# Performance work log

Hardware: AMD Instinct MI355X
Metric: run time of the kernel (lower is better)

The kernel has to match this reference:

```python
import jax, jax.numpy as jnp
import numpy as np

B, C, H, W = 4, 64, 64, 64
NH = 1            # num_heads
HD = C // NH      # head dim
HID = 256         # mlp hidden = 4*dim
EPS = 1e-5


def _gn(x, g, b):
    # GroupNorm with num_groups=1: normalize over (C,H,W) per sample
    mu = x.mean(axis=(1, 2, 3), keepdims=True)
    var = ((x - mu) ** 2).mean(axis=(1, 2, 3), keepdims=True)
    xn = (x - mu) / jnp.sqrt(var + EPS)
    return xn * g[None, :, None, None] + b[None, :, None, None]


def _bn(x, g, b):
    # BatchNorm2d eval mode, running_mean=0, running_var=1
    s = g / jnp.sqrt(1.0 + EPS)
    return x * s[None, :, None, None] + b[None, :, None, None]


def _c1(x, w):
    # 1x1 conv, no bias
    return jnp.einsum('oc,bchw->bohw', w, x)


def _dw(x, w, b):
    # depthwise conv, kernel k, 'same' padding
    k = w.shape[-1]
    p = k // 2
    y = jax.lax.conv_general_dilated(
        x, w, (1, 1), [(p, p), (p, p)],
        dimension_numbers=('NCHW', 'OIHW', 'NCHW'),
        feature_group_count=x.shape[1])
    return y + b[None, :, None, None]


def _rope_sincos():
    d = HD
    angle = 1.0 / 10000 ** jnp.linspace(0.0, 1.0, d // 4)
    angle = jnp.repeat(angle, 2)  # [d/2]
    th = jnp.arange(H, dtype=jnp.float32)[:, None] * angle[None, :]
    tw = jnp.arange(W, dtype=jnp.float32)[:, None] * angle[None, :]
    sin = jnp.concatenate([
        jnp.broadcast_to(jnp.sin(th)[:, None, :], (H, W, d // 2)),
        jnp.broadcast_to(jnp.sin(tw)[None, :, :], (H, W, d // 2))], -1)
    cos = jnp.concatenate([
        jnp.broadcast_to(jnp.cos(th)[:, None, :], (H, W, d // 2)),
        jnp.broadcast_to(jnp.cos(tw)[None, :, :], (H, W, d // 2))], -1)
    return sin.reshape(H * W, d), cos.reshape(H * W, d)


def _rot(x):
    x1 = x[..., ::2]
    x2 = x[..., 1::2]
    return jnp.stack([-x2, x1], axis=-1).reshape(x.shape)


def _theta_shift(x, sin, cos):
    return x * cos + _rot(x) * sin


def _forward(x, cnn_feature, n1_g, n1_b, n2_g, n2_b, n3_g, n3_b,
             q_w, q_b, kv_w, kv_b, lc_w, lc_b,
             fc1_w, bn1_g, bn1_b,
             dw_w1, dw_b1, dw_w3, dw_b3, dw_w5, dw_b5, dw_w7, dw_b7,
             bnm_g, bnm_b, fft_w, fc2_w, bn2_g, bn2_b):
    N = H * W
    sin, cos = _rope_sincos()
    # ---- attention branch ----
    xn = _gn(x, n1_g, n1_b)
    cn = _gn(cnn_feature, n3_g, n3_b)
    q = (_c1(xn, q_w) + q_b[None, :, None, None]).reshape(B, NH, HD, N).transpose(0, 1, 3, 2)
    kv_in = _dw(cn, lc_w, lc_b) + cn          # local_conv(kv) + kv
    kv = _c1(kv_in, kv_w) + kv_b[None, :, None, None]
    k, v = jnp.split(kv, 2, axis=1)
    k = k.reshape(B, NH, HD, N).transpose(0, 1, 3, 2)  # [B,h,N,d]
    v = v.reshape(B, NH, HD, N).transpose(0, 1, 3, 2)
    qr = _theta_shift(q, sin, cos)
    kr = _theta_shift(k, sin, cos)
    attn = jnp.einsum('bhnd,bhmd->bhnm', qr, kr) * (HD ** -0.5)
    attn = jax.nn.softmax(attn, axis=-1)
    o = jnp.einsum('bhnm,bhmd->bhnd', attn, v)
    o = o.transpose(0, 1, 3, 2).reshape(B, C, H, W)
    x = x + o
    # ---- fft MLP branch ----
    xn2 = _gn(x, n2_g, n2_b)
    h = jax.nn.gelu(_bn(_c1(xn2, fc1_w), bn1_g, bn1_b), approximate=False)
    res = h
    c0 = HID - (HID // 4) * 3
    s1, s3, s5, s7 = jnp.split(h, [c0, c0 + HID // 4, c0 + 2 * (HID // 4)], axis=1)
    hd = jnp.concatenate([_dw(s1, dw_w1, dw_b1), _dw(s3, dw_w3, dw_b3),
                          _dw(s5, dw_w5, dw_b5), _dw(s7, dw_w7, dw_b7)], axis=1)
    pad = 0 if W % 2 == 0 else (W // 2 + 1) * 2 - W
    hp = jnp.pad(hd, ((0, 0), (0, 0), (0, 0), (0, pad)))
    hf = jnp.fft.rfft2(hp)
    hf = fft_w * hf
    hp = jnp.fft.irfft2(hf, s=hp.shape[-2:])
    hd = hp[..., :W]
    h = hd + res
    h = _bn(jax.nn.gelu(h, approximate=False), bnm_g, bnm_b)
    out = _bn(_c1(h, fc2_w), bn2_g, bn2_b)
    return x + out


def setup_inputs() -> dict:
    key = jax.random.key(0)
    ks = jax.random.split(key, 16)
    def rn(i, shape, s=0.02):
        return jax.random.normal(ks[i], shape, jnp.float32) * s
    c4 = HID // 4
    c0 = HID - 3 * c4
    return {
        'x': jax.random.normal(ks[0], (B, C, H, W), jnp.float32),
        'cnn_feature': jax.random.normal(ks[1], (B, C, H, W), jnp.float32),
        'n1_g': jnp.ones((C,)), 'n1_b': jnp.zeros((C,)),
        'n2_g': jnp.ones((C,)), 'n2_b': jnp.zeros((C,)),
        'n3_g': jnp.ones((C,)), 'n3_b': jnp.zeros((C,)),
        'q_w': rn(2, (C, C)), 'q_b': jnp.zeros((C,)),
        'kv_w': rn(3, (2 * C, C)), 'kv_b': jnp.zeros((2 * C,)),
        'lc_w': rn(4, (C, 1, 3, 3)), 'lc_b': jnp.zeros((C,)),
        'fc1_w': rn(5, (HID, C)),
        'bn1_g': jnp.ones((HID,)), 'bn1_b': jnp.zeros((HID,)),
        'dw_w1': rn(6, (c0, 1, 1, 1)), 'dw_b1': jnp.zeros((c0,)),
        'dw_w3': rn(7, (c4, 1, 3, 3)), 'dw_b3': jnp.zeros((c4,)),
        'dw_w5': rn(8, (c4, 1, 5, 5)), 'dw_b5': jnp.zeros((c4,)),
        'dw_w7': rn(9, (c4, 1, 7, 7)), 'dw_b7': jnp.zeros((c4,)),
        'bnm_g': jnp.ones((HID,)), 'bnm_b': jnp.zeros((HID,)),
        'fft_w': jax.random.normal(ks[10], (1, HID, 1, 1), jnp.float32),
        'fc2_w': rn(11, (C, HID)),
        'bn2_g': jnp.ones((C,)), 'bn2_b': jnp.zeros((C,)),
    }


def reference(x, cnn_feature, n1_g, n1_b, n2_g, n2_b, n3_g, n3_b,
              q_w, q_b, kv_w, kv_b, lc_w, lc_b,
              fc1_w, bn1_g, bn1_b,
              dw_w1, dw_b1, dw_w3, dw_b3, dw_w5, dw_b5, dw_w7, dw_b7,
              bnm_g, bnm_b, fft_w, fc2_w, bn2_g, bn2_b):
    return _forward(x, cnn_feature, n1_g, n1_b, n2_g, n2_b, n3_g, n3_b,
                    q_w, q_b, kv_w, kv_b, lc_w, lc_b,
                    fc1_w, bn1_g, bn1_b,
                    dw_w1, dw_b1, dw_w3, dw_b3, dw_w5, dw_b5, dw_w7, dw_b7,
                    bnm_g, bnm_b, fft_w, fc2_w, bn2_g, bn2_b)
```

## Files before the change

kernel.cpp:

```cpp
#include <hip/hip_runtime.h>
#include <hip/hip_bf16.h>
#include <math.h>

#define BB 4
#define CC 64
#define NN 4096
#define HD 64
#define HID 256
#define EPSV 1e-5f
#define CNT (CC*NN)
#define NCH 8

typedef float f32x4 __attribute__((ext_vector_type(4)));
typedef short bf16x8 __attribute__((ext_vector_type(8)));
typedef short bf16x4 __attribute__((ext_vector_type(4)));
#define MFMA16(a, b, c) __builtin_amdgcn_mfma_f32_16x16x32_bf16(a, b, c, 0, 0, 0)

__device__ __forceinline__ float gelu_exact(float x) {
    return 0.5f * x * (1.0f + erff(x * 0.70710678118654752f));
}
__device__ __forceinline__ ushort f2bf(float f) {
    unsigned u = __float_as_uint(f);
    unsigned r = (u + 0x7FFFu + ((u >> 16) & 1u)) >> 16;
    return (ushort)r;
}
__device__ __forceinline__ float bf2f(ushort u) {
    return __uint_as_float(((unsigned)u) << 16);
}
__device__ __forceinline__ unsigned cvtpk(float lo, float hi) {
    unsigned r;
    asm("v_cvt_pk_bf16_f32 %0, %1, %2" : "=v"(r) : "v"(lo), "v"(hi));
    return r;
}
__device__ __forceinline__ void unpack2(unsigned u, float& lo, float& hi) {
    lo = __uint_as_float(u << 16);
    hi = __uint_as_float(u & 0xffff0000u);
}

__global__ __launch_bounds__(256) void wprep_kernel(const float* __restrict__ fc1w,
                                                    const float* __restrict__ fc2w,
                                                    const float* __restrict__ qw,
                                                    const float* __restrict__ kvw,
                                                    ushort* __restrict__ fc1wb,
                                                    ushort* __restrict__ fc2wb,
                                                    ushort* __restrict__ qwb,
                                                    ushort* __restrict__ kvwb) {
    int i = blockIdx.x * 256 + threadIdx.x;
    if (i < 16384) fc1wb[i] = f2bf(fc1w[i]);
    else if (i < 32768) fc2wb[i - 16384] = f2bf(fc2w[i - 16384]);
    else if (i < 36864) qwb[i - 32768] = f2bf(qw[i - 32768]);
    else if (i < 45056) kvwb[i - 36864] = f2bf(kvw[i - 36864]);
}

__global__ __launch_bounds__(256) void stats_pair_kernel(const float* __restrict__ x,
                                                         const float* __restrict__ cnn,
                                                         float* __restrict__ part) {
    int b = blockIdx.y;
    int blk = blockIdx.x;
    const float4* p0 = (const float4*)(x + (size_t)b * CNT);
    const float4* p1 = (const float4*)(cnn + (size_t)b * CNT);
    float s0 = 0.f, s20 = 0.f, s1 = 0.f, s21 = 0.f;
    #pragma unroll
    for (int k = 0; k < 4; ++k) {
        float4 v = p0[blk * 1024 + k * 256 + threadIdx.x];
        s0  += v.x + v.y + v.z + v.w;
        s20 += v.x * v.x + v.y * v.y + v.z * v.z + v.w * v.w;
        float4 u = p1[blk * 1024 + k * 256 + threadIdx.x];
        s1  += u.x + u.y + u.z + u.w;
        s21 += u.x * u.x + u.y * u.y + u.z * u.z + u.w * u.w;
    }
    #pragma unroll
    for (int off = 32; off > 0; off >>= 1) {
        s0  += __shfl_xor(s0, off);
        s20 += __shfl_xor(s20, off);
        s1  += __shfl_xor(s1, off);
        s21 += __shfl_xor(s21, off);
    }
    __shared__ float sh[4][4];
    int wid = threadIdx.x >> 6, lane = threadIdx.x & 63;
    if (lane == 0) { sh[wid][0] = s0; sh[wid][1] = s20; sh[wid][2] = s1; sh[wid][3] = s21; }
    __syncthreads();
    if (threadIdx.x == 0) {
        float a0 = sh[0][0] + sh[1][0] + sh[2][0] + sh[3][0];
        float a1 = sh[0][1] + sh[1][1] + sh[2][1] + sh[3][1];
        float a2 = sh[0][2] + sh[1][2] + sh[2][2] + sh[3][2];
        float a3 = sh[0][3] + sh[1][3] + sh[2][3] + sh[3][3];
        part[((0 * 4 + b) * 64 + blk) * 2]     = a0;
        part[((0 * 4 + b) * 64 + blk) * 2 + 1] = a1;
        part[((1 * 4 + b) * 64 + blk) * 2]     = a2;
        part[((1 * 4 + b) * 64 + blk) * 2 + 1] = a3;
    }
}

__global__ __launch_bounds__(64) void stats_fin_kernel(const float* __restrict__ part,
                                                       float* __restrict__ stats) {
    int sb_ = blockIdx.x;
    int lane = threadIdx.x;
    float s = part[(sb_ * 64 + lane) * 2];
    float s2 = part[(sb_ * 64 + lane) * 2 + 1];
    #pragma unroll
    for (int off = 32; off > 0; off >>= 1) {
        s  += __shfl_xor(s, off);
        s2 += __shfl_xor(s2, off);
    }
    if (lane == 0) {
        int slot = sb_ >> 2, b = sb_ & 3;
        float mu = s / (float)CNT;
        float var = s2 / (float)CNT - mu * mu;
        stats[slot * 8 + b] = mu;
        stats[slot * 8 + 4 + b] = rsqrtf(var + EPSV);
    }
}

__global__ __launch_bounds__(256) void stats2b_kernel(const float* __restrict__ part2,
                                                      float* __restrict__ stats, int slot) {
    int b = blockIdx.x;
    int t = threadIdx.x;
    float s = part2[(b * 256 + t) * 2];
    float s2 = part2[(b * 256 + t) * 2 + 1];
    #pragma unroll
    for (int off = 32; off > 0; off >>= 1) {
        s  += __shfl_xor(s, off);
        s2 += __shfl_xor(s2, off);
    }
    __shared__ float shs[4], shs2[4];
    int wid = t >> 6, lane = t & 63;
    if (lane == 0) { shs[wid] = s; shs2[wid] = s2; }
    __syncthreads();
    if (t == 0) {
        float S = shs[0] + shs[1] + shs[2] + shs[3];
        float S2 = shs2[0] + shs2[1] + shs2[2] + shs2[3];
        float mu = S / (float)CNT;
        float var = S2 / (float)CNT - mu * mu;
        stats[slot * 8 + b] = mu;
        stats[slot * 8 + 4 + b] = rsqrtf(var + EPSV);
    }
}

__global__ __launch_bounds__(256) void dw3k_kernel(const float* __restrict__ cnn,
                                                   const float* __restrict__ n3g,
                                                   const float* __restrict__ n3b,
                                                   const float* __restrict__ lcw,
                                                   const float* __restrict__ lcb,
                                                   const float* __restrict__ stats,
                                                   float* __restrict__ kvin) {
    int i = blockIdx.x * 256 + threadIdx.x;
    int x = i & 63;
    int y = (i >> 6) & 63;
    int c = (i >> 12) & 63;
    int b = i >> 18;
    float mu = stats[1 * 8 + b];
    float rs = stats[1 * 8 + 4 + b];
    float sc = rs * n3g[c];
    float of = n3b[c] - mu * sc;
    const float* plane = cnn + ((size_t)(i >> 12) << 12);
    float acc = lcb[c];
    #pragma unroll
    for (int dy = 0; dy < 3; ++dy) {
        int yy = y + dy - 1;
        if (yy < 0 || yy >= 64) continue;
        #pragma unroll
        for (int dx = 0; dx < 3; ++dx) {
            int xx = x + dx - 1;
            if (xx < 0 || xx >= 64) continue;
            acc += lcw[c * 9 + dy * 3 + dx] * (plane[(yy << 6) + xx] * sc + of);
        }
    }
    kvin[i] = acc + plane[(y << 6) + x] * sc + of;
}

__global__ __launch_bounds__(256) void q_mfma(const float* __restrict__ x,
                                              const float* __restrict__ n1g,
                                              const float* __restrict__ n1b,
                                              const ushort* __restrict__ qwb,
                                              const float* __restrict__ qb,
                                              const float* __restrict__ stats,
                                              ushort* __restrict__ qr) {
    int b = blockIdx.y;
    int tok0 = blockIdx.x * 64;
    int tid = threadIdx.x;
    int w = tid >> 6;
    int lr = tid & 15;
    int lg = (tid & 63) >> 4;
    float mu = stats[0 * 8 + b];
    float rs = stats[0 * 8 + 4 + b];
    __shared__ ushort Xt[64][64];
    for (int k = 0; k < 16; ++k) {
        int e = tid + k * 256;
        int c = e >> 6, t = e & 63;
        float v = (x[((size_t)(b * 64 + c)) * NN + tok0 + t] - mu) * rs * n1g[c] + n1b[c];
        Xt[t][((c >> 3) ^ (t & 7)) * 8 + (c & 7)] = f2bf(v);
    }
    __syncthreads();
    int brow = w * 16 + lr;
    bf16x8 bf0 = *(const bf16x8*)&Xt[brow][((0 + lg) ^ (lr & 7)) * 8];
    bf16x8 bf1 = *(const bf16x8*)&Xt[brow][((4 + lg) ^ (lr & 7)) * 8];
    f32x4 acc[4];
    #pragma unroll
    for (int mt = 0; mt < 4; ++mt) acc[mt] = (f32x4){0.f, 0.f, 0.f, 0.f};
    #pragma unroll
    for (int mt = 0; mt < 4; ++mt) {
        bf16x8 a0 = *(const bf16x8*)&qwb[(mt * 16 + lr) * 64 + lg * 8];
        bf16x8 a1 = *(const bf16x8*)&qwb[(mt * 16 + lr) * 64 + 32 + lg * 8];
        acc[mt] = MFMA16(a0, bf0, acc[mt]);
        acc[mt] = MFMA16(a1, bf1, acc[mt]);
    }
    int tok = tok0 + w * 16 + lr;
    int hh = tok >> 6, ww2 = tok & 63;
    ushort* qrow = qr + ((size_t)b * NN + tok) * 64;
    #pragma unroll
    for (int mt = 0; mt < 4; ++mt) {
        #pragma unroll
        for (int pr = 0; pr < 2; ++pr) {
            int o = mt * 16 + lg * 4 + pr * 2;
            float a0 = acc[mt][pr * 2]     + qb[o];
            float a1 = acc[mt][pr * 2 + 1] + qb[o + 1];
            int j = (o & 31) >> 1;
            float freq = exp2f(-0.88584749f * (float)j);
            float pos = (o < 32) ? (float)hh : (float)ww2;
            float st, ct;
            __sincosf(pos * freq, &st, &ct);
            qrow[o]     = f2bf(a0 * ct - a1 * st);
            qrow[o + 1] = f2bf(a1 * ct + a0 * st);
        }
    }
}

__global__ __launch_bounds__(256) void kv_mfma(const float* __restrict__ kvin,
                                               const ushort* __restrict__ kvwb,
                                               const float* __restrict__ kvb,
                                               ushort* __restrict__ kr,
                                               ushort* __restrict__ vt) {
    int b = blockIdx.y;
    int tok0 = blockIdx.x * 64;
    int tid = threadIdx.x;
    int w = tid >> 6;
    int lr = tid & 15;
    int lg = (tid & 63) >> 4;
    __shared__ ushort Xt[64][64];
    for (int k = 0; k < 16; ++k) {
        int e = tid + k * 256;
        int c = e >> 6, t = e & 63;
        Xt[t][((c >> 3) ^ (t & 7)) * 8 + (c & 7)] =
            f2bf(kvin[((size_t)(b * 64 + c)) * NN + tok0 + t]);
    }
    __syncthreads();
    int brow = w * 16 + lr;
    bf16x8 bf0 = *(const bf16x8*)&Xt[brow][((0 + lg) ^ (lr & 7)) * 8];
    bf16x8 bf1 = *(const bf16x8*)&Xt[brow][((4 + lg) ^ (lr & 7)) * 8];
    f32x4 acc[8];
    #pragma unroll
    for (int mt = 0; mt < 8; ++mt) acc[mt] = (f32x4){0.f, 0.f, 0.f, 0.f};
    #pragma unroll
    for (int mt = 0; mt < 8; ++mt) {
        bf16x8 a0 = *(const bf16x8*)&kvwb[(mt * 16 + lr) * 64 + lg * 8];
        bf16x8 a1 = *(const bf16x8*)&kvwb[(mt * 16 + lr) * 64 + 32 + lg * 8];
        acc[mt] = MFMA16(a0, bf0, acc[mt]);
        acc[mt] = MFMA16(a1, bf1, acc[mt]);
    }
    int tl = w * 16 + lr;
    int tok = tok0 + tl;
    int hh = tok >> 6, ww2 = tok & 63;
    int permk = (lr >> 2) * 16 + w * 4 + (lr & 3);
    ushort* krow = kr + ((size_t)b * NN + tok) * 64;
    #pragma unroll
    for (int mt = 0; mt < 4; ++mt) {
        #pragma unroll
        for (int pr = 0; pr < 2; ++pr) {
            int o = mt * 16 + lg * 4 + pr * 2;
            float a0 = acc[mt][pr * 2]     + kvb[o];
            float a1 = acc[mt][pr * 2 + 1] + kvb[o + 1];
            int j = (o & 31) >> 1;
            float freq = exp2f(-0.88584749f * (float)j);
            float pos = (o < 32) ? (float)hh : (float)ww2;
            float st, ct;
            __sincosf(pos * freq, &st, &ct);
            krow[o]     = f2bf(a0 * ct - a1 * st);
            krow[o + 1] = f2bf(a1 * ct + a0 * st);
        }
    }
    #pragma unroll
    for (int mt = 4; mt < 8; ++mt) {
        #pragma unroll
        for (int r = 0; r < 4; ++r) {
            int o = mt * 16 + lg * 4 + r;
            float a0 = acc[mt][r] + kvb[o];
            vt[((size_t)b * 64 + (o - 64)) * NN + tok0 + permk] = f2bf(a0);
        }
    }
}

__global__ __launch_bounds__(256) void attn_kernel(const ushort* __restrict__ qr,
                                                   const ushort* __restrict__ kr,
                                                   const ushort* __restrict__ vt,
                                                   ushort* __restrict__ Opart,
                                                   float* __restrict__ ml) {
    int b = blockIdx.y;
    int q0 = blockIdx.x * 64;
    int chunk = blockIdx.z;
    int tid = threadIdx.x;
    int w = tid >> 6;
    int lane = tid & 63;
    int lr = lane & 15;
    int lg = lane >> 4;
    const float SCL2 = 0.125f * 1.44269504f;

    __shared__ ushort Kl[64 * 64];
    __shared__ ushort Vl[64 * 64];

    bf16x8 qf[2];
    {
        const ushort* qp = qr + ((size_t)b * NN + q0 + w * 16 + lr) * 64;
        qf[0] = *(const bf16x8*)(qp + lg * 8);
        qf[1] = *(const bf16x8*)(qp + 32 + lg * 8);
    }

    f32x4 oacc[4];
    #pragma unroll
    for (int t = 0; t < 4; ++t) oacc[t] = (f32x4){0.f, 0.f, 0.f, 0.f};
    float m_ = -INFINITY, l_ = 0.f;

    const size_t kbase = ((size_t)b * NN) * 64;
    const int t0 = chunk * 8, tend = t0 + 8;

    for (int t = t0; t < tend; ++t) {
        int k0 = t * 64;
        __syncthreads();
        #pragma unroll
        for (int it = 0; it < 2; ++it) {
            int e = tid + it * 256;
            int row = e >> 3, cib = e & 7;
            int sw = cib ^ (row & 7);
            *(bf16x8*)(Kl + row * 64 + sw * 8) =
                *(const bf16x8*)(kr + kbase + (size_t)(k0 + row) * 64 + cib * 8);
            *(bf16x8*)(Vl + row * 64 + sw * 8) =
                *(const bf16x8*)(vt + ((size_t)b * 64 + row) * NN + k0 + cib * 8);
        }
        __syncthreads();

        f32x4 sacc[4];
        #pragma unroll
        for (int kt = 0; kt < 4; ++kt) {
            int row = kt * 16 + lr;
            bf16x8 k0f = *(const bf16x8*)(Kl + row * 64 + ((0 * 4 + lg) ^ (lr & 7)) * 8);
            bf16x8 k1f = *(const bf16x8*)(Kl + row * 64 + ((1 * 4 + lg) ^ (lr & 7)) * 8);
            f32x4 z = {0.f, 0.f, 0.f, 0.f};
            z = MFMA16(k0f, qf[0], z);
            sacc[kt] = MFMA16(k1f, qf[1], z);
        }

        float vmax = fmaxf(fmaxf(fmaxf(sacc[0][0], sacc[0][1]), fmaxf(sacc[0][2], sacc[0][3])),
                           fmaxf(fmaxf(sacc[1][0], sacc[1][1]), fmaxf(sacc[1][2], sacc[1][3])));
        vmax = fmaxf(vmax, fmaxf(fmaxf(fmaxf(sacc[2][0], sacc[2][1]), fmaxf(sacc[2][2], sacc[2][3])),
                                 fmaxf(fmaxf(sacc[3][0], sacc[3][1]), fmaxf(sacc[3][2], sacc[3][3]))));
        vmax = fmaxf(vmax, __shfl_xor(vmax, 16));
        vmax = fmaxf(vmax, __shfl_xor(vmax, 32));
        float mx = vmax * SCL2;
        if (__any(mx - m_ > 8.f)) {
            float mn = fmaxf(m_, mx);
            float cr = exp2f(m_ - mn);
            l_ *= cr;
            m_ = mn;
            float crq[4];
            #pragma unroll
            for (int r = 0; r < 4; ++r) crq[r] = __shfl(cr, lg * 4 + r);
            #pragma unroll
            for (int ht = 0; ht < 4; ++ht)
                #pragma unroll
                for (int r = 0; r < 4; ++r) oacc[ht][r] *= crq[r];
        }

        unsigned u[8];
        float lsum = 0.f;
        #pragma unroll
        for (int kt = 0; kt < 4; ++kt) {
            float p0 = exp2f(sacc[kt][0] * SCL2 - m_);
            float p1 = exp2f(sacc[kt][1] * SCL2 - m_);
            float p2 = exp2f(sacc[kt][2] * SCL2 - m_);
            float p3 = exp2f(sacc[kt][3] * SCL2 - m_);
            lsum += (p0 + p1) + (p2 + p3);
            u[kt * 2]     = cvtpk(p0, p1);
            u[kt * 2 + 1] = cvtpk(p2, p3);
        }
        lsum += __shfl_xor(lsum, 16);
        lsum += __shfl_xor(lsum, 32);
        l_ += lsum;

        uint4 t0v = {u[0], u[1], u[2], u[3]};
        uint4 t1v = {u[4], u[5], u[6], u[7]};
        bf16x8 pa0 = __builtin_bit_cast(bf16x8, t0v);
        bf16x8 pa1 = __builtin_bit_cast(bf16x8, t1v);
        #pragma unroll
        for (int ht = 0; ht < 4; ++ht) {
            int row = ht * 16 + lr;
            bf16x8 vf0 = *(const bf16x8*)(Vl + row * 64 + ((lg * 2) ^ (row & 7)) * 8);
            bf16x8 vf1 = *(const bf16x8*)(Vl + row * 64 + ((lg * 2 + 1) ^ (row & 7)) * 8);
            oacc[ht] = MFMA16(pa0, vf0, oacc[ht]);
            oacc[ht] = MFMA16(pa1, vf1, oacc[ht]);
        }
    }

    int n0 = q0 + w * 16 + lg * 4;
    #pragma unroll
    for (int ht = 0; ht < 4; ++ht) {
        int hd = ht * 16 + lr;
        ushort4 o4;
        o4.x = f2bf(oacc[ht][0]);
        o4.y = f2bf(oacc[ht][1]);
        o4.z = f2bf(oacc[ht][2]);
        o4.w = f2bf(oacc[ht][3]);
        *(ushort4*)&Opart[(((size_t)chunk * BB + b) * 64 + hd) * NN + n0] = o4;
    }
    if (lg == 0) {
        int n = q0 + w * 16 + lr;
        ml[((size_t)b * NN + n) * 16 + chunk * 2]     = m_;
        ml[((size_t)b * NN + n) * 16 + chunk * 2 + 1] = l_;
    }
}

__global__ __launch_bounds__(256) void combine_kernel(const ushort* __restrict__ Opart,
                                                      const float* __restrict__ ml,
                                                      const float* __restrict__ x,
                                                      float* __restrict__ x2,
                                                      float* __restrict__ part2) {
    int i = blockIdx.x * 256 + threadIdx.x;
    int n4 = i & 1023;
    int hd = (i >> 10) & 63;
    int b = i >> 16;
    int n0 = n4 << 2;
    float wgt[4][NCH];
    const float* mlp = ml + ((size_t)b * NN + n0) * 16;
    #pragma unroll
    for (int tk = 0; tk < 4; ++tk) {
        float m[NCH], l[NCH];
        const float4* p4 = (const float4*)(mlp + tk * 16);
        #pragma unroll
        for (int q = 0; q < 4; ++q) {
            float4 v = p4[q];
            m[q * 2] = v.x; l[q * 2] = v.y; m[q * 2 + 1] = v.z; l[q * 2 + 1] = v.w;
        }
        float M = m[0];
        #pragma unroll
        for (int c = 1; c < NCH; ++c) M = fmaxf(M, m[c]);
        float e[NCH], L = 0.f;
        #pragma unroll
        for (int c = 0; c < NCH; ++c) { e[c] = exp2f(m[c] - M); L += l[c] * e[c]; }
        float inv = 1.f / L;
        #pragma unroll
        for (int c = 0; c < NCH; ++c) wgt[tk][c] = e[c] * inv;
    }
    float4 acc = {0.f, 0.f, 0.f, 0.f};
    #pragma unroll
    for (int c = 0; c < NCH; ++c) {
        ushort4 o4 = *(const ushort4*)&Opart[(((size_t)c * BB + b) * 64 + hd) * NN + n0];
        acc.x += bf2f(o4.x) * wgt[0][c];
        acc.y += bf2f(o4.y) * wgt[1][c];
        acc.z += bf2f(o4.z) * wgt[2][c];
        acc.w += bf2f(o4.w) * wgt[3][c];
    }
    size_t off = ((size_t)b * 64 + hd) * NN + n0;
    float4 xv = *(const float4*)&x[off];
    acc.x += xv.x; acc.y += xv.y; acc.z += xv.z; acc.w += xv.w;
    *(float4*)&x2[off] = acc;

    float s = acc.x + acc.y + acc.z + acc.w;
    float s2 = acc.x * acc.x + acc.y * acc.y + acc.z * acc.z + acc.w * acc.w;
    #pragma unroll
    for (int off2 = 32; off2 > 0; off2 >>= 1) {
        s  += __shfl_xor(s, off2);
        s2 += __shfl_xor(s2, off2);
    }
    __shared__ float shs[4], shs2[4];
    int wid = threadIdx.x >> 6, lane = threadIdx.x & 63;
    if (lane == 0) { shs[wid] = s; shs2[wid] = s2; }
    __syncthreads();
    if (threadIdx.x == 0) {
        part2[blockIdx.x * 2]     = shs[0] + shs[1] + shs[2] + shs[3];
        part2[blockIdx.x * 2 + 1] = shs2[0] + shs2[1] + shs2[2] + shs2[3];
    }
}

__global__ __launch_bounds__(256) void fc1_mfma(const float* __restrict__ x2,
                                                const ushort* __restrict__ fc1wb,
                                                const float* __restrict__ n2g,
                                                const float* __restrict__ n2b,
                                                const float* __restrict__ bn1g,
                                                const float* __restrict__ bn1b,
                                                const float* __restrict__ stats,
                                                ushort* __restrict__ h1) {
    int b = blockIdx.y;
    int tok0 = (blockIdx.x >> 1) * 64;
    int half = blockIdx.x & 1;
    int tid = threadIdx.x;
    int w = tid >> 6;
    int lr = tid & 15;
    int lg = (tid & 63) >> 4;
    float mu = stats[2 * 8 + b];
    float rs = stats[2 * 8 + 4 + b];
    __shared__ ushort Xt[64][64];
    for (int k = 0; k < 16; ++k) {
        int e = tid + k * 256;
        int c = e >> 6, t = e & 63;
        float v = (x2[((size_t)(b * 64 + c)) * NN + tok0 + t] - mu) * rs * n2g[c] + n2b[c];
        Xt[t][((c >> 3) ^ (t & 7)) * 8 + (c & 7)] = f2bf(v);
    }
    __syncthreads();
    int brow = w * 16 + lr;
    bf16x8 bf0 = *(const bf16x8*)&Xt[brow][((0 + lg) ^ (lr & 7)) * 8];
    bf16x8 bf1 = *(const bf16x8*)&Xt[brow][((4 + lg) ^ (lr & 7)) * 8];
    f32x4 acc[8];
    #pragma unroll
    for (int mt = 0; mt < 8; ++mt) acc[mt] = (f32x4){0.f, 0.f, 0.f, 0.f};
    const ushort* wb = fc1wb + (size_t)(half * 128) * 64;
    #pragma unroll
    for (int mt = 0; mt < 8; ++mt) {
        bf16x8 a0 = *(const bf16x8*)&wb[(mt * 16 + lr) * 64 + lg * 8];
        bf16x8 a1 = *(const bf16x8*)&wb[(mt * 16 + lr) * 64 + 32 + lg * 8];
        acc[mt] = MFMA16(a0, bf0, acc[mt]);
        acc[mt] = MFMA16(a1, bf1, acc[mt]);
    }
    const float sb = rsqrtf(1.f + EPSV);
    int tok = tok0 + w * 16 + lr;
    #pragma unroll
    for (int mt = 0; mt < 8; ++mt) {
        #pragma unroll
        for (int r = 0; r < 4; ++r) {
            int o = half * 128 + mt * 16 + lg * 4 + r;
            float vv = acc[mt][r] * bn1g[o] * sb + bn1b[o];
            h1[((size_t)b * HID + o) * NN + tok] = f2bf(gelu_exact(vv));
        }
    }
}

__global__ __launch_bounds__(256) void mixer_kernel(const ushort* __restrict__ h1,
                                                    const float* __restrict__ dw1w, const float* __restrict__ dw1b,
                                                    const float* __restrict__ dw3w, const float* __restrict__ dw3b,
                                                    const float* __restrict__ dw5w, const float* __restrict__ dw5b,
                                                    const float* __restrict__ dw7w, const float* __restrict__ dw7b,
                                                    const float* __restrict__ fftw,
                                                    const float* __restrict__ bnmg, const float* __restrict__ bnmb,
                                                    ushort* __restrict__ h2) {
    int c = blockIdx.x >> 1;
    int r0 = (blockIdx.x & 1) * 32;
    int b = blockIdx.y;
    int tid = threadIdx.x;
    __shared__ ushort ls[38][80];
    uint* lz = (uint*)&ls[0][0];
    #pragma unroll
    for (int k = 0; k < 6; ++k) {
        int i = tid + k * 256;
        if (i < 1520) lz[i] = 0;
    }
    __syncthreads();
    const ushort* plane = h1 + (((size_t)b * HID + c) << 12);
    for (int e = tid; e < 304; e += 256) {
        int i = e >> 3, xc = e & 7;
        int gr = r0 + i - 3;
        if (gr >= 0 && gr < 64) {
            bf16x8 v = *(const bf16x8*)&plane[(gr << 6) + xc * 8];
            bf16x4 lo = {v[0], v[1], v[2], v[3]};
            bf16x4 hi = {v[4], v[5], v[6], v[7]};
            *(bf16x4*)&ls[i][xc * 8 + 4] = lo;
            *(bf16x4*)&ls[i][xc * 8 + 8] = hi;
        }
    }
    __syncthreads();

    int yy = tid >> 3;
    int x0 = (tid & 7) * 8;
    const float sb = rsqrtf(1.f + EPSV);
    float fw = fftw[c];
    float bg = bnmg[c] * sb, bb2 = bnmb[c];
    float acc[8], ctr[8];
    #pragma unroll
    for (int j = 0; j < 8; ++j) acc[j] = 0.f;

    if (c < 64) {
        float w0 = dw1w[c], b0 = dw1b[c];
        uint4 ua = *(const uint4*)&ls[yy + 3][x0];
        uint4 ub = *(const uint4*)&ls[yy + 3][x0 + 8];
        float wv[16];
        unpack2(ua.x, wv[0], wv[1]); unpack2(ua.y, wv[2], wv[3]);
        unpack2(ua.z, wv[4], wv[5]); unpack2(ua.w, wv[6], wv[7]);
        unpack2(ub.x, wv[8], wv[9]); unpack2(ub.y, wv[10], wv[11]);
        unpack2(ub.z, wv[12], wv[13]); unpack2(ub.w, wv[14], wv[15]);
        #pragma unroll
        for (int j = 0; j < 8; ++j) { ctr[j] = wv[j + 4]; acc[j] = w0 * ctr[j] + b0; }
    } else if (c < 128) {
        int lc = c - 64;
        float b0 = dw3b[lc];
        #pragma unroll
        for (int j = 0; j < 8; ++j) acc[j] = b0;
        #pragma unroll
        for (int dy = 0; dy < 3; ++dy) {
            int i = yy + dy + 2;
            uint4 ua = *(const uint4*)&ls[i][x0];
            uint4 ub = *(const uint4*)&ls[i][x0 + 8];
            float wv[16];
            unpack2(ua.x, wv[0], wv[1]); unpack2(ua.y, wv[2], wv[3]);
            unpack2(ua.z, wv[4], wv[5]); unpack2(ua.w, wv[6], wv[7]);
            unpack2(ub.x, wv[8], wv[9]); unpack2(ub.y, wv[10], wv[11]);
            unpack2(ub.z, wv[12], wv[13]); unpack2(ub.w, wv[14], wv[15]);
            if (dy == 1) {
                #pragma unroll
                for (int j = 0; j < 8; ++j) ctr[j] = wv[j + 4];
            }
            #pragma unroll
            for (int dx = 0; dx < 3; ++dx) {
                float wt = dw3w[lc * 9 + dy * 3 + dx];
                #pragma unroll
                for (int j = 0; j < 8; ++j) acc[j] += wt * wv[j + dx + 3];
            }
        }
    } else if (c < 192) {
        int lc = c - 128;
        float b0 = dw5b[lc];
        #pragma unroll
        for (int j = 0; j < 8; ++j) acc[j] = b0;
        #pragma unroll
        for (int dy = 0; dy < 5; ++dy) {
            int i = yy + dy + 1;
            uint4 ua = *(const uint4*)&ls[i][x0];
            uint4 ub = *(const uint4*)&ls[i][x0 + 8];
            float wv[16];
            unpack2(ua.x, wv[0], wv[1]); unpack2(ua.y, wv[2], wv[3]);
            unpack2(ua.z, wv[4], wv[5]); unpack2(ua.w, wv[6], wv[7]);
            unpack2(ub.x, wv[8], wv[9]); unpack2(ub.y, wv[10], wv[11]);
            unpack2(ub.z, wv[12], wv[13]); unpack2(ub.w, wv[14], wv[15]);
            if (dy == 2) {
                #pragma unroll
                for (int j = 0; j < 8; ++j) ctr[j] = wv[j + 4];
            }
            #pragma unroll
            for (int dx = 0; dx < 5; ++dx) {
                float wt = dw5w[lc * 25 + dy * 5 + dx];
                #pragma unroll
                for (int j = 0; j < 8; ++j) acc[j] += wt * wv[j + dx + 2];
            }
        }
    } else {
        int lc = c - 192;
        float b0 = dw7b[lc];
        #pragma unroll
        for (int j = 0; j < 8; ++j) acc[j] = b0;
        #pragma unroll
        for (int dy = 0; dy < 7; ++dy) {
            int i = yy + dy;
            uint4 ua = *(const uint4*)&ls[i][x0];
            uint4 ub = *(const uint4*)&ls[i][x0 + 8];
            float wv[16];
            unpack2(ua.x, wv[0], wv[1]); unpack2(ua.y, wv[2], wv[3]);
            unpack2(ua.z, wv[4], wv[5]); unpack2(ua.w, wv[6], wv[7]);
            unpack2(ub.x, wv[8], wv[9]); unpack2(ub.y, wv[10], wv[11]);
            unpack2(ub.z, wv[12], wv[13]); unpack2(ub.w, wv[14], wv[15]);
            if (dy == 3) {
                #pragma unroll
                for (int j = 0; j < 8; ++j) ctr[j] = wv[j + 4];
            }
            #pragma unroll
            for (int dx = 0; dx < 7; ++dx) {
                float wt = dw7w[lc * 49 + dy * 7 + dx];
                #pragma unroll
                for (int j = 0; j < 8; ++j) acc[j] += wt * wv[j + dx + 1];
            }
        }
    }

    bf16x8 o;
    #pragma unroll
    for (int j = 0; j < 8; ++j) {
        float val = fw * acc[j] + ctr[j];
        o[j] = (short)f2bf(gelu_exact(val) * bg + bb2);
    }
    ushort* outp = h2 + (((size_t)b * HID + c) << 12);
    *(bf16x8*)&outp[((r0 + yy) << 6) + x0] = o;
}

__global__ __launch_bounds__(256) void fc2_mfma(const ushort* __restrict__ h2,
                                                const ushort* __restrict__ fc2wb,
                                                const float* __restrict__ bn2g,
                                                const float* __restrict__ bn2b,
                                                const float* __restrict__ x2,
                                                float* __restrict__ out) {
    int b = blockIdx.y;
    int tok0 = blockIdx.x * 64;
    int tid = threadIdx.x;
    int w = tid >> 6;
    int lr = tid & 15;
    int lg = (tid & 63) >> 4;
    __shared__ ushort Xt[64][256];
    for (int k = 0; k < 8; ++k) {
        int e = tid + k * 256;
        int c = e >> 3, t8 = (e & 7) * 8;
        bf16x8 v = *(const bf16x8*)&h2[((size_t)(b * 256 + c)) * NN + tok0 + t8];
        #pragma unroll
        for (int j = 0; j < 8; ++j) {
            int t = t8 + j;
            Xt[t][((c >> 3) ^ (t & 7)) * 8 + (c & 7)] = (ushort)v[j];
        }
    }
    __syncthreads();
    int brow = w * 16 + lr;
    f32x4 acc[4];
    #pragma unroll
    for (int mt = 0; mt < 4; ++mt) acc[mt] = (f32x4){0.f, 0.f, 0.f, 0.f};
    #pragma unroll
    for (int ks = 0; ks < 8; ++ks) {
        bf16x8 bfr = *(const bf16x8*)&Xt[brow][(((ks * 4 + lg) & 7) ^ (lr & 7)) * 8 + ((ks * 4 + lg) & ~7) * 8];
        #pragma unroll
        for (int mt = 0; mt < 4; ++mt) {
            bf16x8 a = *(const bf16x8*)&fc2wb[(mt * 16 + lr) * 256 + ks * 32 + lg * 8];
            acc[mt] = MFMA16(a, bfr, acc[mt]);
        }
    }
    const float sb = rsqrtf(1.f + EPSV);
    int tok = tok0 + w * 16 + lr;
    #pragma unroll
    for (int mt = 0; mt < 4; ++mt) {
        #pragma unroll
        for (int r = 0; r < 4; ++r) {
            int o = mt * 16 + lg * 4 + r;
            size_t off = ((size_t)b * 64 + o) * NN + tok;
            out[off] = acc[mt][r] * bn2g[o] * sb + bn2b[o] + x2[off];
        }
    }
}

extern "C" void kernel_launch(void* const* d_in, const int* in_sizes, int n_in,
                              void* d_out, int out_size, void* d_ws, size_t ws_size,
                              hipStream_t stream) {
    const float* x    = (const float*)d_in[0];
    const float* cnn  = (const float*)d_in[1];
    const float* n1g  = (const float*)d_in[2];
    const float* n1b  = (const float*)d_in[3];
    const float* n2g  = (const float*)d_in[4];
    const float* n2b  = (const float*)d_in[5];
    const float* n3g  = (const float*)d_in[6];
    const float* n3b  = (const float*)d_in[7];
    const float* qw   = (const float*)d_in[8];
    const float* qb   = (const float*)d_in[9];
    const float* kvw  = (const float*)d_in[10];
    const float* kvb  = (const float*)d_in[11];
    const float* lcw  = (const float*)d_in[12];
    const float* lcb  = (const float*)d_in[13];
    const float* fc1w = (const float*)d_in[14];
    const float* bn1g = (const float*)d_in[15];
    const float* bn1b = (const float*)d_in[16];
    const float* dw1w = (const float*)d_in[17];
    const float* dw1b = (const float*)d_in[18];
    const float* dw3w = (const float*)d_in[19];
    const float* dw3b = (const float*)d_in[20];
    const float* dw5w = (const float*)d_in[21];
    const float* dw5b = (const float*)d_in[22];
    const float* dw7w = (const float*)d_in[23];
    const float* dw7b = (const float*)d_in[24];
    const float* bnmg = (const float*)d_in[25];
    const float* bnmb = (const float*)d_in[26];
    const float* fftw = (const float*)d_in[27];
    const float* fc2w = (const float*)d_in[28];
    const float* bn2g = (const float*)d_in[29];
    const float* bn2b = (const float*)d_in[30];

    float* ws = (float*)d_ws;
    float* stats = ws;
    float* part  = ws + 64;
    float* part2 = ws + 1088;
    float* base  = ws + 3200;
    const size_t M = 1048576;
    float* x2     = base;
    ushort* qr_bf = (ushort*)(base + M);
    ushort* kr_bf = (ushort*)(base + M + M / 2);
    ushort* vt_bf = (ushort*)(base + 2 * M);
    float* kvin   = base + 5 * M / 2;
    ushort* Opart = (ushort*)(base + 7 * M / 2);
    float* ml     = base + 15 * M / 2;
    ushort* h1 = (ushort*)(base + M);
    ushort* h2 = (ushort*)(base + 7 * M / 2);
    ushort* fc1wb = (ushort*)(base + 8 * M);
    ushort* fc2wb = fc1wb + 16384;
    ushort* qwb   = fc2wb + 16384;
    ushort* kvwb  = qwb + 4096;
    float* outp = (float*)d_out;

    wprep_kernel<<<176, 256, 0, stream>>>(fc1w, fc2w, qw, kvw, fc1wb, fc2wb, qwb, kvwb);
    stats_pair_kernel<<<dim3(64, 4), 256, 0, stream>>>(x, cnn, part);
    stats_fin_kernel<<<8, 64, 0, stream>>>(part, stats);
    dw3k_kernel<<<4096, 256, 0, stream>>>(cnn, n3g, n3b, lcw, lcb, stats, kvin);
    q_mfma<<<dim3(64, 4), 256, 0, stream>>>(x, n1g, n1b, qwb, qb, stats, qr_bf);
    kv_mfma<<<dim3(64, 4), 256, 0, stream>>>(kvin, kvwb, kvb, kr_bf, vt_bf);
    attn_kernel<<<dim3(64, 4, NCH), 256, 0, stream>>>(qr_bf, kr_bf, vt_bf, Opart, ml);
    combine_kernel<<<1024, 256, 0, stream>>>(Opart, ml, x, x2, part2);
    stats2b_kernel<<<4, 256, 0, stream>>>(part2, stats, 2);
    fc1_mfma<<<dim3(128, 4), 256, 0, stream>>>(x2, fc1wb, n2g, n2b, bn1g, bn1b, stats, h1);
    mixer_kernel<<<dim3(512, 4), 256, 0, stream>>>(h1, dw1w, dw1b, dw3w, dw3b, dw5w, dw5b,
                                                   dw7w, dw7b, fftw, bnmg, bnmb, h2);
    fc2_mfma<<<dim3(64, 4), 256, 0, stream>>>(h2, fc2wb, bn2g, bn2b, x2, outp);
}
```

Baseline: 121.0 us.

## Fuse depthwise 3x3 local conv, Q projection and KV projection into one kernel

```diff
diff --git a/kernel.cpp b/kernel.cpp
--- a/kernel.cpp
+++ b/kernel.cpp
@@ -137,155 +137,159 @@
     }
 }
 
-__global__ __launch_bounds__(256) void dw3k_kernel(const float* __restrict__ cnn,
-                                                   const float* __restrict__ n3g,
-                                                   const float* __restrict__ n3b,
-                                                   const float* __restrict__ lcw,
-                                                   const float* __restrict__ lcb,
-                                                   const float* __restrict__ stats,
-                                                   float* __restrict__ kvin) {
-    int i = blockIdx.x * 256 + threadIdx.x;
-    int x = i & 63;
-    int y = (i >> 6) & 63;
-    int c = (i >> 12) & 63;
-    int b = i >> 18;
-    float mu = stats[1 * 8 + b];
-    float rs = stats[1 * 8 + 4 + b];
-    float sc = rs * n3g[c];
-    float of = n3b[c] - mu * sc;
-    const float* plane = cnn + ((size_t)(i >> 12) << 12);
-    float acc = lcb[c];
-    #pragma unroll
-    for (int dy = 0; dy < 3; ++dy) {
-        int yy = y + dy - 1;
-        if (yy < 0 || yy >= 64) continue;
-        #pragma unroll
-        for (int dx = 0; dx < 3; ++dx) {
-            int xx = x + dx - 1;
-            if (xx < 0 || xx >= 64) continue;
-            acc += lcw[c * 9 + dy * 3 + dx] * (plane[(yy << 6) + xx] * sc + of);
-        }
-    }
-    kvin[i] = acc + plane[(y << 6) + x] * sc + of;
-}
-
-__global__ __launch_bounds__(256) void q_mfma(const float* __restrict__ x,
-                                              const float* __restrict__ n1g,
-                                              const float* __restrict__ n1b,
-                                              const ushort* __restrict__ qwb,
-                                              const float* __restrict__ qb,
-                                              const float* __restrict__ stats,
-                                              ushort* __restrict__ qr) {
+__global__ __launch_bounds__(256) void qkv_fused(const float* __restrict__ x,
+                                                 const float* __restrict__ n1g,
+                                                 const float* __restrict__ n1b,
+                                                 const ushort* __restrict__ qwb,
+                                                 const float* __restrict__ qb,
+                                                 const float* __restrict__ cnn,
+                                                 const float* __restrict__ n3g,
+                                                 const float* __restrict__ n3b,
+                                                 const float* __restrict__ lcw,
+                                                 const float* __restrict__ lcb,
+                                                 const ushort* __restrict__ kvwb,
+                                                 const float* __restrict__ kvb,
+                                                 const float* __restrict__ stats,
+                                                 ushort* __restrict__ qr,
+                                                 ushort* __restrict__ kr,
+                                                 ushort* __restrict__ vt) {
+    int y = blockIdx.x;
     int b = blockIdx.y;
-    int tok0 = blockIdx.x * 64;
     int tid = threadIdx.x;
+    int tok0 = y * 64;
+    __shared__ float cs[3][64][66];
+    __shared__ ushort Xt[64][64];
+    float* csf = &cs[0][0][0];
+    for (int i = tid; i < 3 * 64 * 66; i += 256) csf[i] = 0.f;
+    __syncthreads();
+    {
+        float mu = stats[1 * 8 + b];
+        float rs = stats[1 * 8 + 4 + b];
+        for (int e = tid; e < 12288; e += 256) {
+            int ry = e >> 12;
+            int c = (e >> 6) & 63;
+            int xx = e & 63;
+            int yy = y + ry - 1;
+            if (yy >= 0 && yy < 64)
+                cs[ry][c][xx + 1] =
+                    (cnn[((size_t)(b * 64 + c)) * NN + yy * 64 + xx] - mu) * rs * n3g[c] + n3b[c];
+        }
+    }
+    __syncthreads();
+    {
+        int c = tid >> 2;
+        int x0 = (tid & 3) * 16;
+        float w9[9];
+        #pragma unroll
+        for (int i = 0; i < 9; ++i) w9[i] = lcw[c * 9 + i];
+        float b0 = lcb[c];
+        #pragma unroll
+        for (int px = 0; px < 16; ++px) {
+            int xg = x0 + px;
+            float acc = b0;
+            #pragma unroll
+            for (int dy = 0; dy < 3; ++dy) {
+                const float* row = cs[dy][c];
+                acc += w9[dy * 3]     * row[xg];
+                acc += w9[dy * 3 + 1] * row[xg + 1];
+                acc += w9[dy * 3 + 2] * row[xg + 2];
+            }
+            acc += cs[1][c][xg + 1];
+            Xt[xg][((c >> 3) ^ (xg & 7)) * 8 + (c & 7)] = f2bf(acc);
+        }
+    }
+    __syncthreads();
+
     int w = tid >> 6;
     int lr = tid & 15;
     int lg = (tid & 63) >> 4;
-    float mu = stats[0 * 8 + b];
-    float rs = stats[0 * 8 + 4 + b];
-    __shared__ ushort Xt[64][64];
-    for (int k = 0; k < 16; ++k) {
-        int e = tid + k * 256;
-        int c = e >> 6, t = e & 63;
-        float v = (x[((size_t)(b * 64 + c)) * NN + tok0 + t] - mu) * rs * n1g[c] + n1b[c];
-        Xt[t][((c >> 3) ^ (t & 7)) * 8 + (c & 7)] = f2bf(v);
-    }
-    __syncthreads();
     int brow = w * 16 + lr;
-    bf16x8 bf0 = *(const bf16x8*)&Xt[brow][((0 + lg) ^ (lr & 7)) * 8];
-    bf16x8 bf1 = *(const bf16x8*)&Xt[brow][((4 + lg) ^ (lr & 7)) * 8];
-    f32x4 acc[4];
-    #pragma unroll
-    for (int mt = 0; mt < 4; ++mt) acc[mt] = (f32x4){0.f, 0.f, 0.f, 0.f};
-    #pragma unroll
-    for (int mt = 0; mt < 4; ++mt) {
-        bf16x8 a0 = *(const bf16x8*)&qwb[(mt * 16 + lr) * 64 + lg * 8];
-        bf16x8 a1 = *(const bf16x8*)&qwb[(mt * 16 + lr) * 64 + 32 + lg * 8];
-        acc[mt] = MFMA16(a0, bf0, acc[mt]);
-        acc[mt] = MFMA16(a1, bf1, acc[mt]);
-    }
-    int tok = tok0 + w * 16 + lr;
-    int hh = tok >> 6, ww2 = tok & 63;
-    ushort* qrow = qr + ((size_t)b * NN + tok) * 64;
-    #pragma unroll
-    for (int mt = 0; mt < 4; ++mt) {
-        #pragma unroll
-        for (int pr = 0; pr < 2; ++pr) {
-            int o = mt * 16 + lg * 4 + pr * 2;
-            float a0 = acc[mt][pr * 2]     + qb[o];
-            float a1 = acc[mt][pr * 2 + 1] + qb[o + 1];
-            int j = (o & 31) >> 1;
-            float freq = exp2f(-0.88584749f * (float)j);
-            float pos = (o < 32) ? (float)hh : (float)ww2;
-            float st, ct;
-            __sincosf(pos * freq, &st, &ct);
-            qrow[o]     = f2bf(a0 * ct - a1 * st);
-            qrow[o + 1] = f2bf(a1 * ct + a0 * st);
-        }
-    }
-}
-
-__global__ __launch_bounds__(256) void kv_mfma(const float* __restrict__ kvin,
-                                               const ushort* __restrict__ kvwb,
-                                               const float* __restrict__ kvb,
-                                               ushort* __restrict__ kr,
-                                               ushort* __restrict__ vt) {
-    int b = blockIdx.y;
-    int tok0 = blockIdx.x * 64;
-    int tid = threadIdx.x;
-    int w = tid >> 6;
-    int lr = tid & 15;
-    int lg = (tid & 63) >> 4;
-    __shared__ ushort Xt[64][64];
-    for (int k = 0; k < 16; ++k) {
-        int e = tid + k * 256;
-        int c = e >> 6, t = e & 63;
-        Xt[t][((c >> 3) ^ (t & 7)) * 8 + (c & 7)] =
-            f2bf(kvin[((size_t)(b * 64 + c)) * NN + tok0 + t]);
-    }
-    __syncthreads();
-    int brow = w * 16 + lr;
-    bf16x8 bf0 = *(const bf16x8*)&Xt[brow][((0 + lg) ^ (lr & 7)) * 8];
-    bf16x8 bf1 = *(const bf16x8*)&Xt[brow][((4 + lg) ^ (lr & 7)) * 8];
-    f32x4 acc[8];
-    #pragma unroll
-    for (int mt = 0; mt < 8; ++mt) acc[mt] = (f32x4){0.f, 0.f, 0.f, 0.f};
-    #pragma unroll
-    for (int mt = 0; mt < 8; ++mt) {
-        bf16x8 a0 = *(const bf16x8*)&kvwb[(mt * 16 + lr) * 64 + lg * 8];
-        bf16x8 a1 = *(const bf16x8*)&kvwb[(mt * 16 + lr) * 64 + 32 + lg * 8];
-        acc[mt] = MFMA16(a0, bf0, acc[mt]);
-        acc[mt] = MFMA16(a1, bf1, acc[mt]);
-    }
-    int tl = w * 16 + lr;
-    int tok = tok0 + tl;
-    int hh = tok >> 6, ww2 = tok & 63;
-    int permk = (lr >> 2) * 16 + w * 4 + (lr & 3);
-    ushort* krow = kr + ((size_t)b * NN + tok) * 64;
-    #pragma unroll
-    for (int mt = 0; mt < 4; ++mt) {
-        #pragma unroll
-        for (int pr = 0; pr < 2; ++pr) {
-            int o = mt * 16 + lg * 4 + pr * 2;
-            float a0 = acc[mt][pr * 2]     + kvb[o];
-            float a1 = acc[mt][pr * 2 + 1] + kvb[o + 1];
-            int j = (o & 31) >> 1;
-            float freq = exp2f(-0.88584749f * (float)j);
-            float pos = (o < 32) ? (float)hh : (float)ww2;
-            float st, ct;
-            __sincosf(pos * freq, &st, &ct);
-            krow[o]     = f2bf(a0 * ct - a1 * st);
-            krow[o + 1] = f2bf(a1 * ct + a0 * st);
-        }
-    }
-    #pragma unroll
-    for (int mt = 4; mt < 8; ++mt) {
-        #pragma unroll
-        for (int r = 0; r < 4; ++r) {
-            int o = mt * 16 + lg * 4 + r;
-            float a0 = acc[mt][r] + kvb[o];
-            vt[((size_t)b * 64 + (o - 64)) * NN + tok0 + permk] = f2bf(a0);
+    {
+        bf16x8 bf0 = *(const bf16x8*)&Xt[brow][((0 + lg) ^ (lr & 7)) * 8];
+        bf16x8 bf1 = *(const bf16x8*)&Xt[brow][((4 + lg) ^ (lr & 7)) * 8];
+        f32x4 acc[8];
+        #pragma unroll
+        for (int mt = 0; mt < 8; ++mt) acc[mt] = (f32x4){0.f, 0.f, 0.f, 0.f};
+        #pragma unroll
+        for (int mt = 0; mt < 8; ++mt) {
+            bf16x8 a0 = *(const bf16x8*)&kvwb[(mt * 16 + lr) * 64 + lg * 8];
+            bf16x8 a1 = *(const bf16x8*)&kvwb[(mt * 16 + lr) * 64 + 32 + lg * 8];
+            acc[mt] = MFMA16(a0, bf0, acc[mt]);
+            acc[mt] = MFMA16(a1, bf1, acc[mt]);
+        }
+        int tl = w * 16 + lr;
+        int tok = tok0 + tl;
+        int hh = tok >> 6, ww2 = tok & 63;
+        int permk = (lr >> 2) * 16 + w * 4 + (lr & 3);
+        ushort* krow = kr + ((size_t)b * NN + tok) * 64;
+        #pragma unroll
+        for (int mt = 0; mt < 4; ++mt) {
+            #pragma unroll
+            for (int pr = 0; pr < 2; ++pr) {
+                int o = mt * 16 + lg * 4 + pr * 2;
+                float a0 = acc[mt][pr * 2]     + kvb[o];
+                float a1 = acc[mt][pr * 2 + 1] + kvb[o + 1];
+                int j = (o & 31) >> 1;
+                float freq = exp2f(-0.88584749f * (float)j);
+                float pos = (o < 32) ? (float)hh : (float)ww2;
+                float st, ct;
+                __sincosf(pos * freq, &st, &ct);
+                krow[o]     = f2bf(a0 * ct - a1 * st);
+                krow[o + 1] = f2bf(a1 * ct + a0 * st);
+            }
+        }
+        #pragma unroll
+        for (int mt = 4; mt < 8; ++mt) {
+            #pragma unroll
+            for (int r = 0; r < 4; ++r) {
+                int o = mt * 16 + lg * 4 + r;
+                float a0 = acc[mt][r] + kvb[o];
+                vt[((size_t)b * 64 + (o - 64)) * NN + tok0 + permk] = f2bf(a0);
+            }
+        }
+    }
+    ushort* Xq = (ushort*)csf;
+    {
+        float mu = stats[0 * 8 + b];
+        float rs = stats[0 * 8 + 4 + b];
+        for (int e = tid; e < 4096; e += 256) {
+            int c = e >> 6, t = e & 63;
+            float v = (x[((size_t)(b * 64 + c)) * NN + tok0 + t] - mu) * rs * n1g[c] + n1b[c];
+            Xq[t * 64 + ((c >> 3) ^ (t & 7)) * 8 + (c & 7)] = f2bf(v);
+        }
+    }
+    __syncthreads();
+    {
+        bf16x8 bf0 = *(const bf16x8*)&Xq[brow * 64 + ((0 + lg) ^ (lr & 7)) * 8];
+        bf16x8 bf1 = *(const bf16x8*)&Xq[brow * 64 + ((4 + lg) ^ (lr & 7)) * 8];
+        f32x4 acc[4];
+        #pragma unroll
+        for (int mt = 0; mt < 4; ++mt) acc[mt] = (f32x4){0.f, 0.f, 0.f, 0.f};
+        #pragma unroll
+        for (int mt = 0; mt < 4; ++mt) {
+            bf16x8 a0 = *(const bf16x8*)&qwb[(mt * 16 + lr) * 64 + lg * 8];
+            bf16x8 a1 = *(const bf16x8*)&qwb[(mt * 16 + lr) * 64 + 32 + lg * 8];
+            acc[mt] = MFMA16(a0, bf0, acc[mt]);
+            acc[mt] = MFMA16(a1, bf1, acc[mt]);
+        }
+        int tok = tok0 + w * 16 + lr;
+        int hh = tok >> 6, ww2 = tok & 63;
+        ushort* qrow = qr + ((size_t)b * NN + tok) * 64;
+        #pragma unroll
+        for (int mt = 0; mt < 4; ++mt) {
+            #pragma unroll
+            for (int pr = 0; pr < 2; ++pr) {
+                int o = mt * 16 + lg * 4 + pr * 2;
+                float a0 = acc[mt][pr * 2]     + qb[o];
+                float a1 = acc[mt][pr * 2 + 1] + qb[o + 1];
+                int j = (o & 31) >> 1;
+                float freq = exp2f(-0.88584749f * (float)j);
+                float pos = (o < 32) ? (float)hh : (float)ww2;
+                float st, ct;
+                __sincosf(pos * freq, &st, &ct);
+                qrow[o]     = f2bf(a0 * ct - a1 * st);
+                qrow[o + 1] = f2bf(a1 * ct + a0 * st);
+            }
         }
     }
 }
@@ -771,7 +775,6 @@
     ushort* qr_bf = (ushort*)(base + M);
     ushort* kr_bf = (ushort*)(base + M + M / 2);
     ushort* vt_bf = (ushort*)(base + 2 * M);
-    float* kvin   = base + 5 * M / 2;
     ushort* Opart = (ushort*)(base + 7 * M / 2);
     float* ml     = base + 15 * M / 2;
     ushort* h1 = (ushort*)(base + M);
@@ -785,9 +788,9 @@
     wprep_kernel<<<176, 256, 0, stream>>>(fc1w, fc2w, qw, kvw, fc1wb, fc2wb, qwb, kvwb);
     stats_pair_kernel<<<dim3(64, 4), 256, 0, stream>>>(x, cnn, part);
     stats_fin_kernel<<<8, 64, 0, stream>>>(part, stats);
-    dw3k_kernel<<<4096, 256, 0, stream>>>(cnn, n3g, n3b, lcw, lcb, stats, kvin);
-    q_mfma<<<dim3(64, 4), 256, 0, stream>>>(x, n1g, n1b, qwb, qb, stats, qr_bf);
-    kv_mfma<<<dim3(64, 4), 256, 0, stream>>>(kvin, kvwb, kvb, kr_bf, vt_bf);
+    qkv_fused<<<dim3(64, 4), 256, 0, stream>>>(x, n1g, n1b, qwb, qb, cnn, n3g, n3b,
+                                               lcw, lcb, kvwb, kvb, stats,
+                                               qr_bf, kr_bf, vt_bf);
     attn_kernel<<<dim3(64, 4, NCH), 256, 0, stream>>>(qr_bf, kr_bf, vt_bf, Opart, ml);
     combine_kernel<<<1024, 256, 0, stream>>>(Opart, ml, x, x2, part2);
     stats2b_kernel<<<4, 256, 0, stream>>>(part2, stats, 2);
```

Result: slower. 131.6 us (+8.8%).
